# Kernel optimization log

Measured on AMD Instinct MI355X. Metric: run time of the kernel, lower is better.

The kernel has to match this reference:

```python
import jax, jax.numpy as jnp
import numpy as np

B, S, C, H, E, K = 8, 512, 768, 12, 8, 2
MLP_H = int(C * 4.0)
HD = C // H
ROUTER_REG = 0.01
LN_EPS = 1e-5


def setup_inputs() -> dict:
    key = jax.random.key(0)
    ks = jax.random.split(key, 8)

    def w(k, shape, fan_in):
        return (jax.random.normal(k, shape, dtype=jnp.float32) / np.sqrt(fan_in)).astype(jnp.float32)

    return {
        "x": jax.random.normal(ks[0], (B, S, C), dtype=jnp.float32),
        "expert_tokens": w(ks[1], (E, C), C),
        "ln1_g": jnp.ones((E, C), jnp.float32),
        "ln1_b": jnp.zeros((E, C), jnp.float32),
        "qkv_w": w(ks[2], (E, C, 3 * C), C),
        "qkv_b": jnp.zeros((E, 3 * C), jnp.float32),
        "proj_w": w(ks[3], (E, C, C), C),
        "proj_b": jnp.zeros((E, C), jnp.float32),
        "ln2_g": jnp.ones((E, C), jnp.float32),
        "ln2_b": jnp.zeros((E, C), jnp.float32),
        "fc1_w": w(ks[4], (E, C, MLP_H), C),
        "fc1_b": jnp.zeros((E, MLP_H), jnp.float32),
        "fc2_w": w(ks[5], (E, MLP_H, C), MLP_H),
        "fc2_b": jnp.zeros((E, C), jnp.float32),
    }


def _layernorm(x, g, b):
    mu = jnp.mean(x, axis=-1, keepdims=True)
    var = jnp.mean(jnp.square(x - mu), axis=-1, keepdims=True)
    return (x - mu) * jax.lax.rsqrt(var + LN_EPS) * g + b


def _block(x, p):
    # One transformer Block (pre-LN attention + MLP), params for a single expert.
    ln1_g, ln1_b, qkv_w, qkv_b, proj_w, proj_b, ln2_g, ln2_b, fc1_w, fc1_b, fc2_w, fc2_b = p
    h = _layernorm(x, ln1_g, ln1_b)
    qkv = (h @ qkv_w + qkv_b).reshape(B, S, 3, H, HD)
    q, k, v = qkv[:, :, 0], qkv[:, :, 1], qkv[:, :, 2]  # [B,S,H,HD]
    # NOTE: original code MULTIPLIES by sqrt(head_dim) (scale = head_dim**0.5).
    scale = jnp.float32(np.sqrt(HD))
    attn = jax.nn.softmax(jnp.einsum('bqhd,bkhd->bhqk', q, k) * scale, axis=-1)
    o = jnp.einsum('bhqk,bkhd->bqhd', attn, v).reshape(B, S, C)
    x = x + (o @ proj_w + proj_b)
    h2 = _layernorm(x, ln2_g, ln2_b)
    x = x + (jax.nn.gelu(h2 @ fc1_w + fc1_b, approximate=False) @ fc2_w + fc2_b)
    return x


def reference(x, expert_tokens, ln1_g, ln1_b, qkv_w, qkv_b, proj_w, proj_b,
              ln2_g, ln2_b, fc1_w, fc1_b, fc2_w, fc2_b):
    # Router
    router_logits = jnp.einsum('bsc,nc->bsn', x, expert_tokens) / jnp.float32(np.sqrt(C))
    router_probs = jax.nn.softmax(router_logits, axis=-1)
    top_k_probs, top_k_idx = jax.lax.top_k(router_probs, K)  # [B,S,K]
    top_k_probs = top_k_probs / jnp.sum(top_k_probs, axis=-1, keepdims=True)

    # Dense all-expert compute (sequential over experts to bound memory)
    params = (ln1_g, ln1_b, qkv_w, qkv_b, proj_w, proj_b, ln2_g, ln2_b,
              fc1_w, fc1_b, fc2_w, fc2_b)
    expert_out = jax.lax.map(lambda p: _block(x, p), params)  # [E,B,S,C]
    expert_out = jnp.transpose(expert_out, (1, 2, 0, 3))       # [B,S,E,C]

    # Top-k gather and weighted combine
    sel = jnp.take_along_axis(expert_out, top_k_idx[..., None], axis=2)  # [B,S,K,C]
    combine = jnp.sum(sel * top_k_probs[..., None], axis=2)
    out = x + combine

    # Load-balance auxiliary loss
    counts = jnp.sum(jax.nn.one_hot(top_k_idx, E, dtype=jnp.float32), axis=(0, 1, 2))
    f_i = counts / jnp.float32(B * S * K)
    P_i = jnp.mean(router_probs, axis=(0, 1))
    balance_loss = E * jnp.sum(f_i * P_i) + ROUTER_REG * jnp.linalg.norm(expert_tokens)
    return out, balance_loss
```

## Files before the change

### kernel.cpp

```cpp
#include <hip/hip_runtime.h>
#include <hip/hip_bf16.h>

#define BB 8
#define SS 512
#define CC 768
#define HH 12
#define HD 64
#define EE 8
#define KK 2
#define MLPH 3072
#define NT (BB*SS)
#define NOUT (NT*CC)

#define SLOTB      68059136ull
#define SLOT_U16   34029568ull
#define SLOT_F32   17014784ull

typedef unsigned int u32;
typedef unsigned short u16;
typedef __attribute__((ext_vector_type(8))) short short8;
typedef __attribute__((ext_vector_type(4))) float f32x4;

__device__ __forceinline__ u16 f2bf(float f) {
    u32 u = __builtin_bit_cast(u32, f);
    u32 r = (u + 0x7fffu + ((u >> 16) & 1u)) >> 16;
    return (u16)r;
}
__device__ __forceinline__ float bf2f(u16 h) {
    u32 u = ((u32)h) << 16;
    return __builtin_bit_cast(float, u);
}
__device__ __forceinline__ void gl_lds16(const void* g, void* l) {
    __builtin_amdgcn_global_load_lds(
        (const __attribute__((address_space(1))) u32*)g,
        (__attribute__((address_space(3))) u32*)l, 16, 0, 0);
}
__device__ __forceinline__ void swz_rc(int bid, int& bm, int& bn) {
    int xcd = bid & 7, off = bid >> 3;
    bm = (xcd * 4 + (off & 3)) * 128;
    bn = (off >> 2) * 128;
}

__device__ __forceinline__ void stage128x64(const u16* __restrict__ G, size_t ldg,
                                            u16* s, int tid)
{
    int wid = tid >> 6, lane = tid & 63;
#pragma unroll
    for (int it = 0; it < 4; ++it) {
        int cb = it * 256 + wid * 64;
        int c = cb + lane;
        int row = c >> 3;
        int ch = (c & 7) ^ (row & 7);
        gl_lds16(G + (size_t)row * ldg + ch * 8, s + cb * 8);
    }
}
__device__ __forceinline__ short8 frag64(const u16* s, int row, int kc, int lb) {
    int ch = (kc * 4 + lb) ^ (row & 7);
    return *(const short8*)(s + row * 64 + ch * 8);
}

__global__ __launch_bounds__(256) void router_kernel(const float* __restrict__ x,
    const float* __restrict__ et, float* __restrict__ W, float* __restrict__ stats)
{
    __shared__ float etl[EE * CC];
    __shared__ float pred[4][2 * EE];
    int tid = threadIdx.x;
    for (int i = tid; i < EE * CC; i += 256) etl[i] = et[i];
    __syncthreads();
    int wid = tid >> 6, lane = tid & 63;
    float psum[EE] = {}, csum[EE] = {};
    for (int i = 0; i < 2; i++) {
        int t = blockIdx.x * 8 + wid * 2 + i;
        const float* xr = x + (size_t)t * CC;
        float acc[EE] = {};
        for (int c = lane; c < CC; c += 64) {
            float xv = xr[c];
#pragma unroll
            for (int e = 0; e < EE; e++) acc[e] += xv * etl[e * CC + c];
        }
#pragma unroll
        for (int e = 0; e < EE; e++)
            for (int off = 1; off < 64; off <<= 1) acc[e] += __shfl_xor(acc[e], off, 64);
        if (lane == 0) {
            const float inv = 0.03608439182435161f;
            float l[EE], m = -1e30f;
#pragma unroll
            for (int e = 0; e < EE; e++) { l[e] = acc[e] * inv; m = fmaxf(m, l[e]); }
            float p[EE], sum = 0.f;
#pragma unroll
            for (int e = 0; e < EE; e++) { p[e] = __expf(l[e] - m); sum += p[e]; }
            int i1 = 0;
#pragma unroll
            for (int e = 1; e < EE; e++) if (p[e] > p[i1]) i1 = e;
            int i2 = -1;
#pragma unroll
            for (int e = 0; e < EE; e++) if (e != i1 && (i2 < 0 || p[e] > p[i2])) i2 = e;
            float wn = p[i1] + p[i2];
#pragma unroll
            for (int e = 0; e < EE; e++) W[t * EE + e] = 0.f;
            W[t * EE + i1] = p[i1] / wn;
            W[t * EE + i2] = p[i2] / wn;
#pragma unroll
            for (int e = 0; e < EE; e++) psum[e] += p[e] / sum;
            csum[i1] += 1.f; csum[i2] += 1.f;
        }
    }
    if (lane == 0) {
#pragma unroll
        for (int e = 0; e < EE; e++) { pred[wid][e] = psum[e]; pred[wid][EE + e] = csum[e]; }
    }
    __syncthreads();
    if (tid < 2 * EE) {
        float s = pred[0][tid] + pred[1][tid] + pred[2][tid] + pred[3][tid];
        atomicAdd(&stats[tid], s);
    }
}

template<int MODE>
__global__ __launch_bounds__(256) void ln_kernel(const float* __restrict__ x, size_t xslot,
    u16* __restrict__ out_hi, u16* __restrict__ out_lo, size_t oslot)
{
    int t = blockIdx.x;
    int eb = blockIdx.y;
    const float* xr = x + (size_t)eb * xslot + (size_t)t * CC;
    __shared__ float red[256];
    int tid = threadIdx.x;
    float v[3];
    float s = 0.f;
#pragma unroll
    for (int i = 0; i < 3; i++) { v[i] = xr[tid + i * 256]; s += v[i]; }
    red[tid] = s; __syncthreads();
    for (int off = 128; off > 0; off >>= 1) { if (tid < off) red[tid] += red[tid + off]; __syncthreads(); }
    float mu = red[0] / (float)CC;
    __syncthreads();
    float s2 = 0.f;
#pragma unroll
    for (int i = 0; i < 3; i++) { float d = v[i] - mu; s2 += d * d; }
    red[tid] = s2; __syncthreads();
    for (int off = 128; off > 0; off >>= 1) { if (tid < off) red[tid] += red[tid + off]; __syncthreads(); }
    float var = red[0] / (float)CC;
    float sc = rsqrtf(var + 1e-5f);
#pragma unroll
    for (int i = 0; i < 3; i++) {
        int c = tid + i * 256;
        float val = (v[i] - mu) * sc;
        u16 hi = f2bf(val);
        out_hi[(size_t)eb * oslot + (size_t)t * CC + c] = hi;
        if (MODE) out_lo[(size_t)eb * oslot + (size_t)t * CC + c] = f2bf(val - bf2f(hi));
    }
}

__global__ __launch_bounds__(256) void prep_expert(
    const float* __restrict__ qkv_w0, const float* __restrict__ qkv_b0,
    const float* __restrict__ proj_w0,
    const float* __restrict__ fc1_w0, const float* __restrict__ fc1_b0,
    const float* __restrict__ fc2_w0,
    const float* __restrict__ g1_0, const float* __restrict__ b1_0,
    const float* __restrict__ g2_0, const float* __restrict__ b2_0,
    u16* __restrict__ qkvTh, u16* __restrict__ qkvTl,
    u16* __restrict__ projT, u16* __restrict__ fc1T, u16* __restrict__ fc2T,
    float* __restrict__ biasq, float* __restrict__ biasf1, int ebase)
{
    __shared__ float tile[32][33];
    __shared__ float bsh[CC];
    __shared__ float redg[256];
    int bid = blockIdx.x;
    int eb = blockIdx.y;
    int ge = ebase + eb;
    int tid = threadIdx.x;
    const float* qkv_w = qkv_w0 + (size_t)ge * CC * 3 * CC;
    const float* qkv_b = qkv_b0 + (size_t)ge * 3 * CC;
    const float* proj_w = proj_w0 + (size_t)ge * CC * CC;
    const float* fc1_w = fc1_w0 + (size_t)ge * CC * MLPH;
    const float* fc1_b = fc1_b0 + (size_t)ge * MLPH;
    const float* fc2_w = fc2_w0 + (size_t)ge * MLPH * CC;
    const float* g1 = g1_0 + (size_t)ge * CC;
    const float* b1 = b1_0 + (size_t)ge * CC;
    const float* g2 = g2_0 + (size_t)ge * CC;
    const float* b2 = b2_0 + (size_t)ge * CC;

    if (bid < 6912) {
        const float* src; const float* scale = nullptr;
        u16 *dh, *dl = nullptr; int N, Kd, n0, k0;
        if (bid < 1728) {
            src = qkv_w; scale = g1;
            dh = qkvTh + (size_t)eb * SLOT_U16; dl = qkvTl + (size_t)eb * SLOT_U16;
            N = 2304; Kd = 768; n0 = (bid % 72) * 32; k0 = (bid / 72) * 32;
        } else if (bid < 2304) {
            int i = bid - 1728;
            src = proj_w; dh = projT + (size_t)eb * SLOT_U16; N = 768; Kd = 768;
            n0 = (i % 24) * 32; k0 = (i / 24) * 32;
        } else if (bid < 4608) {
            int i = bid - 2304;
            src = fc1_w; scale = g2; dh = fc1T + (size_t)eb * SLOT_U16; N = 3072; Kd = 768;
            n0 = (i % 96) * 32; k0 = (i / 96) * 32;
        } else {
            int i = bid - 4608;
            src = fc2_w; dh = fc2T + (size_t)eb * SLOT_U16; N = 768; Kd = 3072;
            n0 = (i % 24) * 32; k0 = (i / 24) * 32;
        }
        int tx = tid & 31, ty = tid >> 5;
#pragma unroll
        for (int i = 0; i < 32; i += 8) {
            float v = src[(size_t)(k0 + ty + i) * N + n0 + tx];
            if (scale) v *= scale[k0 + ty + i];
            tile[ty + i][tx] = v;
        }
        __syncthreads();
#pragma unroll
        for (int i = 0; i < 32; i += 8) {
            float v = tile[tx][ty + i];
            u16 hi = f2bf(v);
            dh[(size_t)(n0 + ty + i) * Kd + k0 + tx] = hi;
            if (dl) dl[(size_t)(n0 + ty + i) * Kd + k0 + tx] = f2bf(v - bf2f(hi));
        }
    } else {
        const float* bv; const float* wsrc; const float* badd;
        float* dst; int N, n0;
        if (bid < 6984) { bv = b1; wsrc = qkv_w; badd = qkv_b; dst = biasq + (size_t)eb * SLOT_F32; N = 2304; n0 = (bid - 6912) * 32; }
        else            { bv = b2; wsrc = fc1_w; badd = fc1_b; dst = biasf1 + (size_t)eb * SLOT_F32; N = MLPH; n0 = (bid - 6984) * 32; }
        for (int i = tid; i < CC; i += 256) bsh[i] = bv[i];
        __syncthreads();
        int g = tid & 31, l8 = tid >> 5;
        int n = n0 + g;
        float acc = 0.f;
        for (int k = l8; k < CC; k += 8) acc += bsh[k] * wsrc[(size_t)k * N + n];
        redg[tid] = acc; __syncthreads();
        if (tid < 32) {
            float sum = 0.f;
#pragma unroll
            for (int i = 0; i < 8; i++) sum += redg[tid + i * 32];
            dst[n0 + tid] = sum + badd[n0 + tid];
        }
    }
}

__global__ __launch_bounds__(256) void gemm_qkv_bk64(
    const u16* __restrict__ Ah, const u16* __restrict__ Al,
    const u16* __restrict__ Bh0, const u16* __restrict__ Bl0,
    const float* __restrict__ biasq0, u16* __restrict__ qk_hi0,
    u16* __restrict__ qk_lo0, u16* __restrict__ vtout0)
{
    __shared__ __align__(16) u16 sAh[128 * 64], sAl[128 * 64];
    __shared__ __align__(16) u16 sBh[128 * 64], sBl[128 * 64];
    int tid = threadIdx.x;
    int eb = blockIdx.y;
    int bm, bn;
    swz_rc(blockIdx.x, bm, bn);
    bool qk_tile = (bn < 1536);
    int wid = tid >> 6, lane = tid & 63;
    int wr = wid >> 1, wc = wid & 1;
    int la = lane & 15, lb = lane >> 4;
    const u16* Bh = Bh0 + (size_t)eb * SLOT_U16;
    const u16* Bl = Bl0 + (size_t)eb * SLOT_U16;
    const float* bias = biasq0 + (size_t)eb * SLOT_F32;
    u16* qk_hi = qk_hi0 + (size_t)eb * SLOT_U16;
    u16* qk_lo = qk_lo0 + (size_t)eb * SLOT_U16;
    u16* vtout = vtout0 + (size_t)eb * SLOT_U16;

    f32x4 acc[4][4];
#pragma unroll
    for (int i = 0; i < 4; i++)
#pragma unroll
        for (int j = 0; j < 4; j++) acc[i][j] = (f32x4){0.f, 0.f, 0.f, 0.f};

    const u16* Abh = Ah + (size_t)bm * CC;
    const u16* Abl = Al + (size_t)bm * CC;
    const u16* Bbh = Bh + (size_t)bn * CC;
    const u16* Bbl = Bl + (size_t)bn * CC;
    for (int k0 = 0; k0 < CC; k0 += 64) {
        stage128x64(Abh + k0, CC, sAh, tid);
        stage128x64(Bbh + k0, CC, sBh, tid);
        if (qk_tile) {
            stage128x64(Abl + k0, CC, sAl, tid);
            stage128x64(Bbl + k0, CC, sBl, tid);
        }
        __syncthreads();
        if (qk_tile) {
#pragma unroll
            for (int kc = 0; kc < 2; kc++) {
                short8 avh[4], avl[4], bvh[4], bvl[4];
#pragma unroll
                for (int i = 0; i < 4; i++) {
                    int row = wr * 64 + i * 16 + la;
                    avh[i] = frag64(sAh, row, kc, lb);
                    avl[i] = frag64(sAl, row, kc, lb);
                }
#pragma unroll
                for (int j = 0; j < 4; j++) {
                    int row = wc * 64 + j * 16 + la;
                    bvh[j] = frag64(sBh, row, kc, lb);
                    bvl[j] = frag64(sBl, row, kc, lb);
                }
#pragma unroll
                for (int i = 0; i < 4; i++)
#pragma unroll
                    for (int j = 0; j < 4; j++) {
                        acc[i][j] = __builtin_amdgcn_mfma_f32_16x16x32_bf16(avh[i], bvh[j], acc[i][j], 0, 0, 0);
                        acc[i][j] = __builtin_amdgcn_mfma_f32_16x16x32_bf16(avh[i], bvl[j], acc[i][j], 0, 0, 0);
                        acc[i][j] = __builtin_amdgcn_mfma_f32_16x16x32_bf16(avl[i], bvh[j], acc[i][j], 0, 0, 0);
                    }
            }
        } else {
#pragma unroll
            for (int kc = 0; kc < 2; kc++) {
                short8 avh[4], bvh[4];
#pragma unroll
                for (int i = 0; i < 4; i++) avh[i] = frag64(sAh, wr * 64 + i * 16 + la, kc, lb);
#pragma unroll
                for (int j = 0; j < 4; j++) bvh[j] = frag64(sBh, wc * 64 + j * 16 + la, kc, lb);
#pragma unroll
                for (int i = 0; i < 4; i++)
#pragma unroll
                    for (int j = 0; j < 4; j++)
                        acc[i][j] = __builtin_amdgcn_mfma_f32_16x16x32_bf16(avh[i], bvh[j], acc[i][j], 0, 0, 0);
            }
        }
        __syncthreads();
    }
#pragma unroll
    for (int i = 0; i < 4; i++) {
#pragma unroll
        for (int j = 0; j < 4; j++) {
            int gn = bn + wc * 64 + j * 16 + la;
            float bsv = bias[gn];
#pragma unroll
            for (int r = 0; r < 4; r++) {
                int gm = bm + wr * 64 + i * 16 + lb * 4 + r;
                float v = acc[i][j][r] + bsv;
                if (gn < 1536) {
                    u16 hi = f2bf(v);
                    qk_hi[(size_t)gm * 1536 + gn] = hi;
                    qk_lo[(size_t)gm * 1536 + gn] = f2bf(v - bf2f(hi));
                } else {
                    int dd = (gn - 1536) & 63, hh = (gn - 1536) >> 6;
                    int ss = gm & (SS - 1), bb = gm >> 9;
                    vtout[((size_t)((bb * HH + hh) * HD + dd)) * SS + ss] = f2bf(v);
                }
            }
        }
    }
}

template<int EPI>
__global__ __launch_bounds__(256) void gemm_b(
    const u16* __restrict__ A, size_t Aslot,
    const u16* __restrict__ BT, size_t Bslot,
    const float* __restrict__ bias, size_t biasSlot,
    const float* __restrict__ res, size_t resSlot,
    const float* __restrict__ Wt, int ebase,
    const float* __restrict__ xinit,
    void* __restrict__ Cout, size_t CoutSlot, int N, int Kdim)
{
    __shared__ __align__(16) u16 sA[128 * 64];
    __shared__ __align__(16) u16 sB[128 * 64];
    int tid = threadIdx.x;
    int eb = blockIdx.y;
    int ge = ebase + eb;
    int bm, bn;
    swz_rc(blockIdx.x, bm, bn);
    int wid = tid >> 6, lane = tid & 63;
    int wr = wid >> 1, wc = wid & 1;
    int la = lane & 15, lb = lane >> 4;
    f32x4 acc[4][4];
#pragma unroll
    for (int i = 0; i < 4; i++)
#pragma unroll
        for (int j = 0; j < 4; j++) acc[i][j] = (f32x4){0.f, 0.f, 0.f, 0.f};

    const u16* Ab = A + (size_t)eb * Aslot + (size_t)bm * Kdim;
    const u16* Bb = BT + (size_t)eb * Bslot + (size_t)bn * Kdim;
    for (int k0 = 0; k0 < Kdim; k0 += 64) {
        stage128x64(Ab + k0, Kdim, sA, tid);
        stage128x64(Bb + k0, Kdim, sB, tid);
        __syncthreads();
#pragma unroll
        for (int kc = 0; kc < 2; kc++) {
            short8 av[4], bv[4];
#pragma unroll
            for (int i = 0; i < 4; i++) av[i] = frag64(sA, wr * 64 + i * 16 + la, kc, lb);
#pragma unroll
            for (int j = 0; j < 4; j++) bv[j] = frag64(sB, wc * 64 + j * 16 + la, kc, lb);
#pragma unroll
            for (int i = 0; i < 4; i++)
#pragma unroll
                for (int j = 0; j < 4; j++)
                    acc[i][j] = __builtin_amdgcn_mfma_f32_16x16x32_bf16(av[i], bv[j], acc[i][j], 0, 0, 0);
        }
        __syncthreads();
    }
    const float* biasp = bias + (size_t)eb * biasSlot;
    const float* resp = res ? res + (size_t)eb * resSlot : nullptr;
#pragma unroll
    for (int i = 0; i < 4; i++) {
#pragma unroll
        for (int j = 0; j < 4; j++) {
            int gn = bn + wc * 64 + j * 16 + la;
            float bsv = biasp[gn];
#pragma unroll
            for (int r = 0; r < 4; r++) {
                int gm = bm + wr * 64 + i * 16 + lb * 4 + r;
                size_t idx = (size_t)gm * N + gn;
                float v = acc[i][j][r];
                if (EPI == 1) {
                    ((float*)Cout + (size_t)eb * CoutSlot)[idx] = resp[idx] + v + bsv;
                } else if (EPI == 2) {
                    v += bsv;
                    float gel = 0.5f * v * (1.0f + erff(v * 0.70710678118654752f));
                    ((u16*)Cout + (size_t)eb * CoutSlot)[idx] = f2bf(gel);
                } else {
                    float w = Wt[(size_t)gm * EE + ge];
                    float val = w * (v + bsv + resp[idx]);
                    if (ge == 0) val += xinit[idx];
                    atomicAdd(&((float*)Cout)[idx], val);
                }
            }
        }
    }
}

__global__ __launch_bounds__(256) void attn_mfma(const u16* __restrict__ qk_hi0,
    const u16* __restrict__ qk_lo0, const u16* __restrict__ vt0, u16* __restrict__ o0)
{
    int q0 = blockIdx.x * 64;
    int h = blockIdx.y;
    int z = blockIdx.z;
    int b = z & (BB - 1), eb = z >> 3;
    int tid = threadIdx.x, wid = tid >> 6, lane = tid & 63;
    int la = lane & 15, lb = lane >> 4;
    __shared__ __align__(16) u16 Ksh[64 * 64];
    __shared__ __align__(16) u16 Ksl[64 * 64];
    __shared__ __align__(16) u16 Vs[64 * 64];
    __shared__ __align__(16) u16 Ps[4][16 * 64];

    const u16* qk_hi = qk_hi0 + (size_t)eb * SLOT_U16;
    const u16* qk_lo = qk_lo0 + (size_t)eb * SLOT_U16;
    const u16* vt = vt0 + (size_t)eb * SLOT_U16;
    u16* o = o0 + (size_t)eb * SLOT_U16;

    short8 aqh[2], aql[2];
    {
        size_t qoff = (size_t)(b * SS + q0 + wid * 16 + la) * 1536 + h * HD;
#pragma unroll
        for (int kc = 0; kc < 2; kc++) {
            aqh[kc] = *(const short8*)(qk_hi + qoff + kc * 32 + lb * 8);
            aql[kc] = *(const short8*)(qk_lo + qoff + kc * 32 + lb * 8);
        }
    }
    const u16* kbh = qk_hi + (size_t)(b * SS) * 1536 + CC + h * HD;
    const u16* kbl = qk_lo + (size_t)(b * SS) * 1536 + CC + h * HD;
    const u16* vtbase = vt + (size_t)((b * HH + h) * HD) * SS;

    float m_r[4], l_r[4];
    f32x4 acc_o[4];
#pragma unroll
    for (int r = 0; r < 4; r++) { m_r[r] = -1e30f; l_r[r] = 0.f; }
#pragma unroll
    for (int d0 = 0; d0 < 4; d0++) acc_o[d0] = (f32x4){0.f, 0.f, 0.f, 0.f};

    for (int kt = 0; kt < SS; kt += 64) {
#pragma unroll
        for (int it = 0; it < 2; it++) {
            int base = it * 256 + wid * 64;
            int c = base + lane;
            int row = c >> 3;
            int gk = (c & 7) ^ (row & 7);
            gl_lds16(kbh + (size_t)(kt + row) * 1536 + gk * 8, Ksh + base * 8);
            gl_lds16(kbl + (size_t)(kt + row) * 1536 + gk * 8, Ksl + base * 8);
            gl_lds16(vtbase + (size_t)row * SS + kt + gk * 8, Vs + base * 8);
        }
        __syncthreads();

        f32x4 s4[4];
#pragma unroll
        for (int j = 0; j < 4; j++) s4[j] = (f32x4){0.f, 0.f, 0.f, 0.f};
#pragma unroll
        for (int kc = 0; kc < 2; kc++)
#pragma unroll
            for (int j = 0; j < 4; j++) {
                size_t off = (size_t)(j * 16 + la) * 64 + (((kc * 4 + lb) ^ (la & 7)) * 8);
                short8 bkh = *(const short8*)(Ksh + off);
                short8 bkl = *(const short8*)(Ksl + off);
                s4[j] = __builtin_amdgcn_mfma_f32_16x16x32_bf16(aqh[kc], bkh, s4[j], 0, 0, 0);
                s4[j] = __builtin_amdgcn_mfma_f32_16x16x32_bf16(aql[kc], bkh, s4[j], 0, 0, 0);
                s4[j] = __builtin_amdgcn_mfma_f32_16x16x32_bf16(aqh[kc], bkl, s4[j], 0, 0, 0);
            }
#pragma unroll
        for (int j = 0; j < 4; j++) s4[j] = s4[j] * 8.f;

#pragma unroll
        for (int r = 0; r < 4; r++) {
            float mx = fmaxf(fmaxf(s4[0][r], s4[1][r]), fmaxf(s4[2][r], s4[3][r]));
#pragma unroll
            for (int off = 1; off < 16; off <<= 1) mx = fmaxf(mx, __shfl_xor(mx, off, 64));
            float mn = fmaxf(m_r[r], mx);
            float corr = __expf(m_r[r] - mn);
            m_r[r] = mn;
            float rs = 0.f;
#pragma unroll
            for (int j = 0; j < 4; j++) {
                float p = __expf(s4[j][r] - mn);
                s4[j][r] = p; rs += p;
            }
#pragma unroll
            for (int off = 1; off < 16; off <<= 1) rs += __shfl_xor(rs, off, 64);
            l_r[r] = l_r[r] * corr + rs;
#pragma unroll
            for (int d0 = 0; d0 < 4; d0++) acc_o[d0][r] = acc_o[d0][r] * corr;
        }
#pragma unroll
        for (int j = 0; j < 4; j++)
#pragma unroll
            for (int r = 0; r < 4; r++) {
                int row = lb * 4 + r;
                int sg = (2 * j + (la >> 3)) ^ (row & 7);
                Ps[wid][row * 64 + sg * 8 + (la & 7)] = f2bf(s4[j][r]);
            }
        short8 pa[2];
#pragma unroll
        for (int kc = 0; kc < 2; kc++)
            pa[kc] = *(const short8*)(&Ps[wid][la * 64 + (((kc * 4 + lb) ^ (la & 7)) * 8)]);
#pragma unroll
        for (int d0 = 0; d0 < 4; d0++)
#pragma unroll
            for (int kc = 0; kc < 2; kc++) {
                short8 bv = *(const short8*)(&Vs[(d0 * 16 + la) * 64 + (((kc * 4 + lb) ^ (la & 7)) * 8)]);
                acc_o[d0] = __builtin_amdgcn_mfma_f32_16x16x32_bf16(pa[kc], bv, acc_o[d0], 0, 0, 0);
            }
        __syncthreads();
    }
#pragma unroll
    for (int r = 0; r < 4; r++) {
        float invl = 1.f / l_r[r];
        int tok = b * SS + q0 + wid * 16 + lb * 4 + r;
#pragma unroll
        for (int d0 = 0; d0 < 4; d0++)
            o[(size_t)tok * CC + h * HD + d0 * 16 + la] = f2bf(acc_o[d0][r] * invl);
    }
}

__global__ __launch_bounds__(256) void loss_kernel(const float* __restrict__ et,
    const float* __restrict__ stats, float* __restrict__ out_loss)
{
    __shared__ float red[256];
    int tid = threadIdx.x;
    float s = 0.f;
    for (int i = tid; i < EE * CC; i += 256) { float v = et[i]; s += v * v; }
    red[tid] = s; __syncthreads();
    for (int off = 128; off > 0; off >>= 1) { if (tid < off) red[tid] += red[tid + off]; __syncthreads(); }
    if (tid == 0) {
        float bl = 0.f;
        for (int e = 0; e < EE; e++) {
            float f = stats[EE + e] / (float)(NT * KK);
            float P = stats[e] / (float)NT;
            bl += f * P;
        }
        *out_loss = (float)EE * bl + 0.01f * sqrtf(red[0]);
    }
}

extern "C" void kernel_launch(void* const* d_in, const int* in_sizes, int n_in,
                              void* d_out, int out_size, void* d_ws, size_t ws_size,
                              hipStream_t stream) {
    const float* x      = (const float*)d_in[0];
    const float* et     = (const float*)d_in[1];
    const float* ln1_g  = (const float*)d_in[2];
    const float* ln1_b  = (const float*)d_in[3];
    const float* qkv_w  = (const float*)d_in[4];
    const float* qkv_b  = (const float*)d_in[5];
    const float* proj_w = (const float*)d_in[6];
    const float* proj_b = (const float*)d_in[7];
    const float* ln2_g  = (const float*)d_in[8];
    const float* ln2_b  = (const float*)d_in[9];
    const float* fc1_w  = (const float*)d_in[10];
    const float* fc1_b  = (const float*)d_in[11];
    const float* fc2_w  = (const float*)d_in[12];
    const float* fc2_b  = (const float*)d_in[13];
    float* outp = (float*)d_out;
    char* base = (char*)d_ws;

    const size_t FIXED = 12714496;
    int EB = 1;
    if (ws_size >= FIXED + 8 * SLOTB) EB = 8;
    else if (ws_size >= FIXED + 4 * SLOTB) EB = 4;
    else if (ws_size >= FIXED + 2 * SLOTB) EB = 2;

    float* W      = (float*)(base);
    float* stats  = (float*)(base + 131072);
    u16*   xh_hi  = (u16*)  (base + 131584);
    u16*   xh_lo  = (u16*)  (base + 6423040);
    char* slot0 = base + FIXED;
    u16*   qkvTh  = (u16*)  (slot0);
    u16*   qkvTl  = (u16*)  (slot0 + 3538944);
    u16*   projT  = (u16*)  (slot0 + 7077888);
    u16*   fc1T   = (u16*)  (slot0 + 8257536);
    u16*   fc2T   = (u16*)  (slot0 + 12976128);
    float* biasq  = (float*)(slot0 + 17694720);
    float* biasf1 = (float*)(slot0 + 17711104);
    u16*   qk_hi  = (u16*)  (slot0 + 17727488);
    u16*   qk_lo  = (u16*)  (slot0 + 30310400);
    u16*   mlp1   = (u16*)  (slot0 + 17727488);
    u16*   vtb    = (u16*)  (slot0 + 42893312);
    u16*   xmhat  = (u16*)  (slot0 + 42893312);
    u16*   obf    = (u16*)  (slot0 + 49184768);
    float* xmid   = (float*)(slot0 + 55476224);

    hipMemsetAsync(stats, 0, 16 * sizeof(float), stream);
    hipMemsetAsync(outp, 0, (size_t)NOUT * sizeof(float), stream);

    router_kernel<<<NT / 8, 256, 0, stream>>>(x, et, W, stats);
    ln_kernel<1><<<dim3(NT, 1), 256, 0, stream>>>(x, 0, xh_hi, xh_lo, 0);

    for (int ebase = 0; ebase < EE; ebase += EB) {
        prep_expert<<<dim3(7080, EB), 256, 0, stream>>>(
            qkv_w, qkv_b, proj_w, fc1_w, fc1_b, fc2_w,
            ln1_g, ln1_b, ln2_g, ln2_b,
            qkvTh, qkvTl, projT, fc1T, fc2T, biasq, biasf1, ebase);

        gemm_qkv_bk64<<<dim3(18 * 32, EB), 256, 0, stream>>>(
            xh_hi, xh_lo, qkvTh, qkvTl, biasq, qk_hi, qk_lo, vtb);

        attn_mfma<<<dim3(SS / 64, HH, BB * EB), 256, 0, stream>>>(qk_hi, qk_lo, vtb, obf);

        gemm_b<1><<<dim3(6 * 32, EB), 256, 0, stream>>>(
            obf, SLOT_U16, projT, SLOT_U16, proj_b + (size_t)ebase * CC, CC,
            x, 0, nullptr, 0, nullptr, xmid, SLOT_F32, CC, CC);

        ln_kernel<0><<<dim3(NT, EB), 256, 0, stream>>>(xmid, SLOT_F32, xmhat, nullptr, SLOT_U16);

        gemm_b<2><<<dim3(24 * 32, EB), 256, 0, stream>>>(
            xmhat, SLOT_U16, fc1T, SLOT_U16, biasf1, SLOT_F32,
            nullptr, 0, nullptr, 0, nullptr, mlp1, SLOT_U16, MLPH, CC);

        gemm_b<5><<<dim3(6 * 32, EB), 256, 0, stream>>>(
            mlp1, SLOT_U16, fc2T, SLOT_U16, fc2_b + (size_t)ebase * CC, CC,
            xmid, SLOT_F32, W, ebase, x, outp, 0, CC, MLPH);
    }

    loss_kernel<<<1, 256, 0, stream>>>(et, stats, outp + NOUT);
}
```

Before: 1.566 ms.

## Add dedicated 256x256-tile triple-buffered fc1 GEMM with fused GELU

Replaces the generic gemm_b<2> used for the fc1 projection with a specialised kernel. It uses 512 threads, a 256x256 output tile and a BK=32 triple-buffered LDS pipeline fed by direct global-to-LDS loads. Blocks are remapped so neighbouring tiles land on the same XCD, and s_setprio is raised around the MFMA section. The intent is better operand reuse and latency hiding on the largest GEMM, at the cost of heavy register pressure from 32 accumulators per lane and lower occupancy.

```diff
diff --git a/kernel.cpp b/kernel.cpp
--- a/kernel.cpp
+++ b/kernel.cpp
@@ -404,16 +404,101 @@
                 float v = acc[i][j][r];
                 if (EPI == 1) {
                     ((float*)Cout + (size_t)eb * CoutSlot)[idx] = resp[idx] + v + bsv;
-                } else if (EPI == 2) {
-                    v += bsv;
-                    float gel = 0.5f * v * (1.0f + erff(v * 0.70710678118654752f));
-                    ((u16*)Cout + (size_t)eb * CoutSlot)[idx] = f2bf(gel);
                 } else {
                     float w = Wt[(size_t)gm * EE + ge];
                     float val = w * (v + bsv + resp[idx]);
                     if (ge == 0) val += xinit[idx];
                     atomicAdd(&((float*)Cout)[idx], val);
                 }
+            }
+        }
+    }
+}
+
+__global__ __launch_bounds__(512, 2) void gemm_fc1_p(
+    const u16* __restrict__ A0, const u16* __restrict__ BT0,
+    const float* __restrict__ bias0, u16* __restrict__ C0)
+{
+    __shared__ __align__(16) u16 sA[3][256 * 32];
+    __shared__ __align__(16) u16 sB[3][256 * 32];
+    const int NTILE = CC / 32;
+    int tid = threadIdx.x;
+    int eb = blockIdx.y;
+    int xcd = blockIdx.x & 7, off = blockIdx.x >> 3;
+    int lid = xcd * 24 + off;
+    int bn = (lid / 16) * 256;
+    int bm = (lid % 16) * 256;
+    int wid = tid >> 6, lane = tid & 63;
+    int wm = wid >> 2, wn = wid & 3;
+    int la = lane & 15, lb = lane >> 4;
+
+    const u16* Ab = A0 + (size_t)eb * SLOT_U16 + (size_t)bm * CC;
+    const u16* Bb = BT0 + (size_t)eb * SLOT_U16 + (size_t)bn * CC;
+
+    auto STG = [&](int s, int t) {
+#pragma unroll
+        for (int rd = 0; rd < 2; rd++) {
+            int cb = rd * 512 + wid * 64;
+            int c = cb + lane;
+            gl_lds16(Ab + (size_t)(c >> 2) * CC + t * 32 + (c & 3) * 8, &sA[s][(size_t)cb * 8]);
+        }
+#pragma unroll
+        for (int rd = 0; rd < 2; rd++) {
+            int cb = rd * 512 + wid * 64;
+            int c = cb + lane;
+            gl_lds16(Bb + (size_t)(c >> 2) * CC + t * 32 + (c & 3) * 8, &sB[s][(size_t)cb * 8]);
+        }
+    };
+
+    f32x4 acc[8][4];
+#pragma unroll
+    for (int i = 0; i < 8; i++)
+#pragma unroll
+        for (int j = 0; j < 4; j++) acc[i][j] = (f32x4){0.f, 0.f, 0.f, 0.f};
+
+    STG(0, 0);
+    STG(1, 1);
+
+    for (int t = 0; t < NTILE; t++) {
+        if (t < NTILE - 1) asm volatile("s_waitcnt vmcnt(4)" ::: "memory");
+        else               asm volatile("s_waitcnt vmcnt(0)" ::: "memory");
+        asm volatile("" ::: "memory");
+        __builtin_amdgcn_s_barrier();
+        asm volatile("" ::: "memory");
+
+        const u16* cA = &sA[t % 3][0];
+        const u16* cB = &sB[t % 3][0];
+        __builtin_amdgcn_s_setprio(1);
+        short8 bfr[4];
+#pragma unroll
+        for (int j = 0; j < 4; j++)
+            bfr[j] = *(const short8*)(cB + ((size_t)(wn * 64 + j * 16 + la) * 4 + lb) * 8);
+#pragma unroll
+        for (int i = 0; i < 8; i++) {
+            short8 af = *(const short8*)(cA + ((size_t)(wm * 128 + i * 16 + la) * 4 + lb) * 8);
+#pragma unroll
+            for (int j = 0; j < 4; j++)
+                acc[i][j] = __builtin_amdgcn_mfma_f32_16x16x32_bf16(af, bfr[j], acc[i][j], 0, 0, 0);
+        }
+        __builtin_amdgcn_s_setprio(0);
+
+        if (t + 2 < NTILE) STG((t + 2) % 3, t + 2);
+    }
+
+    const float* bp = bias0 + (size_t)eb * SLOT_F32;
+    u16* C = C0 + (size_t)eb * SLOT_U16;
+#pragma unroll
+    for (int i = 0; i < 8; i++) {
+#pragma unroll
+        for (int j = 0; j < 4; j++) {
+            int gn = bn + wn * 64 + j * 16 + la;
+            float bsv = bp[gn];
+#pragma unroll
+            for (int r = 0; r < 4; r++) {
+                int gm = bm + wm * 128 + i * 16 + lb * 4 + r;
+                float v = acc[i][j][r] + bsv;
+                float gel = 0.5f * v * (1.0f + erff(v * 0.70710678118654752f));
+                C[(size_t)gm * MLPH + gn] = f2bf(gel);
             }
         }
     }
@@ -628,9 +713,7 @@
 
         ln_kernel<0><<<dim3(NT, EB), 256, 0, stream>>>(xmid, SLOT_F32, xmhat, nullptr, SLOT_U16);
 
-        gemm_b<2><<<dim3(24 * 32, EB), 256, 0, stream>>>(
-            xmhat, SLOT_U16, fc1T, SLOT_U16, biasf1, SLOT_F32,
-            nullptr, 0, nullptr, 0, nullptr, mlp1, SLOT_U16, MLPH, CC);
+        gemm_fc1_p<<<dim3(192, EB), 512, 0, stream>>>(xmhat, fc1T, biasf1, mlp1);
 
         gemm_b<5><<<dim3(6 * 32, EB), 256, 0, stream>>>(
             mlp1, SLOT_U16, fc2T, SLOT_U16, fc2_b + (size_t)ebase * CC, CC,
```

Result: slower. 1.598 ms (+2.0%).
